# Optimization experiments

Hardware: AMD Instinct MI355X
Metric: run time of the kernel (lower is better)

## Reference

```python
import jax, jax.numpy as jnp
import numpy as np

DT_MIN, DT_MAX = 1e-3, 0.1
DT_RANK, D_STATE, D_CONV = 64, 16, 4


def setup_inputs() -> dict:
    key = jax.random.key(0)
    ks = jax.random.split(key, 8)
    B, T, Dm = 4, 4096, 1024
    Dn = 2 * Dm  # expand * d_model
    s = lambda k, shape, scale=0.02: (jax.random.normal(k, shape, jnp.float32) * scale)
    return {
        "x": jax.random.normal(ks[0], (B, T, Dm), jnp.float32),
        "W_in": s(ks[1], (2 * Dn, Dm)),
        "conv_w": s(ks[2], (Dn, 1, D_CONV), 0.1),
        "conv_b": jnp.zeros((Dn,), jnp.float32),
        "W_x": s(ks[3], (DT_RANK + 2 * D_STATE, Dn)),
        "W_dt": s(ks[4], (Dn, DT_RANK)),
        "b_dt": jnp.zeros((Dn,), jnp.float32),
        "log_A": jax.random.uniform(ks[5], (Dn, D_STATE), jnp.float32),
        "D_param": jnp.ones((Dn,), jnp.float32),
        "W_out": s(ks[6], (Dm, Dn)),
        "ln_w": jnp.ones((Dm,), jnp.float32),
        "ln_b": jnp.zeros((Dm,), jnp.float32),
    }


def reference(x, W_in, conv_w, conv_b, W_x, W_dt, b_dt, log_A, D_param, W_out, ln_w, ln_b):
    B, T, Dm = x.shape
    Dn = W_dt.shape[0]
    residual = x
    # LayerNorm (biased variance, eps=1e-5, as torch)
    mu = x.mean(-1, keepdims=True)
    var = x.var(-1, keepdims=True)
    xn = (x - mu) / jnp.sqrt(var + 1e-5) * ln_w + ln_b
    # in_proj -> split into x_inner, z
    xz = xn @ W_in.T  # (B,T,2*Dn)
    x_inner, z = jnp.split(xz, 2, axis=-1)
    # causal depthwise conv (torch pads both sides d_conv-1 then slices [:T] == left-pad only)
    xc = jnp.transpose(x_inner, (0, 2, 1))  # (B,Dn,T)
    xc = jax.lax.conv_general_dilated(
        xc, conv_w, window_strides=(1,), padding=[(D_CONV - 1, 0)],
        dimension_numbers=("NCH", "OIH", "NCH"), feature_group_count=Dn)
    xc = xc + conv_b[None, :, None]
    u = jax.nn.silu(jnp.transpose(xc, (0, 2, 1)))  # (B,T,Dn)
    # input-dependent dt, B, C
    xbc = u @ W_x.T
    dt_low, B_ssm, C_ssm = jnp.split(xbc, [DT_RANK, DT_RANK + D_STATE], axis=-1)
    dt = jax.nn.softplus(dt_low @ W_dt.T + b_dt) + DT_MIN
    dt = jnp.clip(dt, DT_MIN, DT_MAX)  # (B,T,Dn)
    A = -jnp.exp(log_A)  # (Dn,N), always negative -> stable
    # selective scan: h_t = exp(dt*A)*h_{t-1} + (dt*u)*B_t ; y_t = <C_t, h_t>
    def step(h, inp):
        dt_t, u_t, B_t, C_t = inp  # (B,Dn),(B,Dn),(B,N),(B,N)
        dA = jnp.exp(dt_t[:, :, None] * A)  # (B,Dn,N)
        h = dA * h + (dt_t * u_t)[:, :, None] * B_t[:, None, :]
        y = jnp.einsum("bdn,bn->bd", h, C_t)
        return h, y

    h0 = jnp.zeros((B, Dn, D_STATE), x.dtype)
    _, ys = jax.lax.scan(
        step, h0,
        (jnp.moveaxis(dt, 1, 0), jnp.moveaxis(u, 1, 0),
         jnp.moveaxis(B_ssm, 1, 0), jnp.moveaxis(C_ssm, 1, 0)))
    y = jnp.moveaxis(ys, 0, 1)  # (B,T,Dn)
    y = y + u * D_param
    y = y * jax.nn.silu(z)
    return y @ W_out.T + residual
```

## Files before the change

kernel.cpp:

```cpp
#include <hip/hip_runtime.h>
#include <cstdint>
#include <cstddef>

#define TT 4096
#define DM 1024
#define DN 2048
#define MROWS 16384
#define NCH 64
#define CHL 64
#define SW 16
#define XBCS 128

typedef unsigned short u16;
typedef u16 ushort8_t __attribute__((ext_vector_type(8)));
typedef u16 ushort4_t __attribute__((ext_vector_type(4)));
typedef short bf16x8 __attribute__((ext_vector_type(8)));
typedef float f32x4 __attribute__((ext_vector_type(4)));

#define EXP2(x) __builtin_amdgcn_exp2f(x)
#define L2E 1.44269504f

__device__ __forceinline__ float bf2f(u16 b) {
  return __uint_as_float(((unsigned int)b) << 16);
}
__device__ __forceinline__ u16 f2bf(float f) {
  unsigned int u = __float_as_uint(f);
  u = u + 0x7FFFu + ((u >> 16) & 1u);
  return (u16)(u >> 16);
}
__device__ __forceinline__ u16 f2h(float f) {
  _Float16 h = (_Float16)f;
  return __builtin_bit_cast(u16, h);
}
__device__ __forceinline__ float h2f(u16 v) {
  return (float)__builtin_bit_cast(_Float16, v);
}

__device__ __forceinline__ void gload_lds16(const void* g, void* l) {
  __builtin_amdgcn_global_load_lds(
      (const __attribute__((address_space(1))) unsigned int*)g,
      (__attribute__((address_space(3))) unsigned int*)l, 16, 0, 0);
}

#define FENCE() asm volatile("" ::: "memory")

__global__ __launch_bounds__(256) void cvt_bf16_kernel(const float* __restrict__ in,
    u16* __restrict__ out, int n4) {
  int i = blockIdx.x * 256 + threadIdx.x;
  if (i >= n4) return;
  float4 v = ((const float4*)in)[i];
  ushort4_t o; o[0] = f2bf(v.x); o[1] = f2bf(v.y); o[2] = f2bf(v.z); o[3] = f2bf(v.w);
  ((ushort4_t*)out)[i] = o;
}

__global__ __launch_bounds__(256) void cvt_wx_kernel(const float* __restrict__ W_x,
    u16* __restrict__ out) {
  int i = blockIdx.x * 256 + threadIdx.x;
  int row = i >> 9;
  ushort4_t o;
  if (row < 96) {
    float4 v = ((const float4*)W_x)[i];
    o[0] = f2bf(v.x); o[1] = f2bf(v.y); o[2] = f2bf(v.z); o[3] = f2bf(v.w);
  } else {
    o[0] = 0; o[1] = 0; o[2] = 0; o[3] = 0;
  }
  ((ushort4_t*)out)[i] = o;
}

__global__ __launch_bounds__(256) void ln_kernel(const float* __restrict__ x,
    const float* __restrict__ ln_w, const float* __restrict__ ln_b,
    u16* __restrict__ xn) {
  int row = blockIdx.x;
  int tid = threadIdx.x;
  const float4* xr = (const float4*)(x + (size_t)row * DM);
  float4 v = xr[tid];
  float s  = v.x + v.y + v.z + v.w;
  float s2 = v.x*v.x + v.y*v.y + v.z*v.z + v.w*v.w;
#pragma unroll
  for (int o = 32; o > 0; o >>= 1) { s += __shfl_down(s, o, 64); s2 += __shfl_down(s2, o, 64); }
  __shared__ float red[2][4];
  __shared__ float mv[2];
  int wid = tid >> 6, lane = tid & 63;
  if (lane == 0) { red[0][wid] = s; red[1][wid] = s2; }
  __syncthreads();
  if (tid == 0) {
    float a  = red[0][0] + red[0][1] + red[0][2] + red[0][3];
    float b2 = red[1][0] + red[1][1] + red[1][2] + red[1][3];
    float mean = a * (1.f / DM);
    float var  = b2 * (1.f / DM) - mean * mean;
    mv[0] = mean; mv[1] = rsqrtf(var + 1e-5f);
  }
  __syncthreads();
  float mean = mv[0], inv = mv[1];
  float4 w = ((const float4*)ln_w)[tid];
  float4 b = ((const float4*)ln_b)[tid];
  ushort4_t o;
  o[0] = f2bf((v.x - mean) * inv * w.x + b.x);
  o[1] = f2bf((v.y - mean) * inv * w.y + b.y);
  o[2] = f2bf((v.z - mean) * inv * w.z + b.z);
  o[3] = f2bf((v.w - mean) * inv * w.w + b.w);
  *(ushort4_t*)(xn + (size_t)row * DM + tid * 4) = o;
}

template<int MODE>
__global__ __launch_bounds__(256) void gemm_mfma_nt(
    const u16* __restrict__ A, int lda,
    const u16* __restrict__ B, int ldb,
    void* __restrict__ Cp, int ldc,
    const float* __restrict__ Res, int K,
    const float* __restrict__ bias, u16* __restrict__ dl_out) {
  __shared__ __align__(16) u16 a_s[128 * 64];
  __shared__ __align__(16) u16 b_s[128 * 64];
  const int tid = threadIdx.x;
  const int w = tid >> 6, l = tid & 63;
  const int wr = w >> 1, wc = w & 1;
  const int nbx = gridDim.x, gy = gridDim.y;
  int lin = blockIdx.y * nbx + blockIdx.x;
  int xcd = lin & 7;
  int m = lin >> 3;
  int bi, bj;
  if (gy >= 8) {
    int njx = gy >> 3;
    bi = m / njx;
    bj = xcd * njx + m % njx;
  } else {
    int cpx = (nbx * gy) >> 3;
    int swz = xcd * cpx + m;
    bi = swz % nbx; bj = swz / nbx;
  }
  const int lrow = l >> 3;
  const int scol = ((l & 7) ^ lrow) * 16;

  f32x4 acc[4][4] = {};

  const int brow = (MODE == 4) ? 0 : bj;
  const u16* Abase = A + (size_t)(bi * 128 + w * 8 + lrow) * lda;
  const u16* Bbase = B + (size_t)(brow * 128 + w * 8 + lrow) * ldb;

  int kbeg = 0, kend = K;
  if constexpr (MODE == 4) { kbeg = bj * (K >> 1); kend = kbeg + (K >> 1); }
  for (int k0 = kbeg; k0 < kend; k0 += 64) {
#pragma unroll
    for (int c = 0; c < 4; c++) {
      const char* ga = (const char*)(Abase + (size_t)(c * 32) * lda + k0) + scol;
      const char* gb = (const char*)(Bbase + (size_t)(c * 32) * ldb + k0) + scol;
      gload_lds16(ga, (char*)a_s + c * 4096 + w * 1024);
      gload_lds16(gb, (char*)b_s + c * 4096 + w * 1024);
    }
    __syncthreads();
#pragma unroll
    for (int kk = 0; kk < 2; kk++) {
      bf16x8 af[4], bfr[4];
#pragma unroll
      for (int m2 = 0; m2 < 4; m2++) {
        int fr = wr * 64 + m2 * 16 + (l & 15);
        int cb = (kk * 64 + ((l >> 4) << 4)) ^ ((fr & 7) << 4);
        af[m2] = *(const bf16x8*)((const char*)a_s + fr * 128 + cb);
      }
#pragma unroll
      for (int n = 0; n < 4; n++) {
        int fr = wc * 64 + n * 16 + (l & 15);
        int cb = (kk * 64 + ((l >> 4) << 4)) ^ ((fr & 7) << 4);
        bfr[n] = *(const bf16x8*)((const char*)b_s + fr * 128 + cb);
      }
#pragma unroll
      for (int m2 = 0; m2 < 4; m2++)
#pragma unroll
        for (int n = 0; n < 4; n++)
          acc[m2][n] = __builtin_amdgcn_mfma_f32_16x16x32_bf16(af[m2], bfr[n], acc[m2][n], 0, 0, 0);
    }
    __syncthreads();
  }
  const int col0 = ((MODE == 4) ? 0 : bj * 128) + wc * 64 + (l & 15);
  const int row0 = bi * 128 + wr * 64 + (l >> 4) * 4;
#pragma unroll
  for (int m2 = 0; m2 < 4; m2++)
#pragma unroll
    for (int n = 0; n < 4; n++) {
      int col = col0 + n * 16;
      float bv = 0.f;
      if constexpr (MODE == 3) bv = bias[col];
#pragma unroll
      for (int r = 0; r < 4; r++) {
        size_t row = (size_t)(row0 + m2 * 16 + r);
        float v = acc[m2][n][r];
        if constexpr (MODE == 0) {
          ((u16*)Cp)[row * ldc + col] = f2bf(v);
        } else if constexpr (MODE == 2) {
          v += Res[row * ldc + col];
          ((float*)Cp)[row * ldc + col] = v;
        } else if constexpr (MODE == 4) {
          ((float*)Cp)[(size_t)bj * ((size_t)MROWS * 128) + row * ldc + col] = v;
        } else {
          float s = v + bv;
          float sp = __logf(1.f + __expf(s));
          float dtv = fminf(sp + 1e-3f, 0.1f);
          ((u16*)Cp)[row * ldc + col] = f2h(dtv);
        }
      }
    }
}

__global__ __launch_bounds__(256) void xbc_merge(const float* __restrict__ p0,
    const float* __restrict__ p1, float* __restrict__ xbc, u16* __restrict__ dl) {
  int i = blockIdx.x * 256 + threadIdx.x;
  float4 a = ((const float4*)p0)[i];
  float4 b = ((const float4*)p1)[i];
  float4 s; s.x = a.x + b.x; s.y = a.y + b.y; s.z = a.z + b.z; s.w = a.w + b.w;
  ((float4*)xbc)[i] = s;
  int col = (i & 31) * 4;
  if (col < 64) {
    int row = i >> 5;
    ushort4_t o; o[0] = f2bf(s.x); o[1] = f2bf(s.y); o[2] = f2bf(s.z); o[3] = f2bf(s.w);
    *(ushort4_t*)(dl + (size_t)row * 64 + col) = o;
  }
}

template<int MODE>
__global__ __launch_bounds__(512) void gemm256(
    const u16* __restrict__ A, int lda,
    const u16* __restrict__ B, int ldb,
    void* __restrict__ Cp, int ldc,
    const float* __restrict__ Res, int K) {
  extern __shared__ char smem[];
  const int tid = threadIdx.x;
  const int w = tid >> 6, l = tid & 63;
  const int wm = w >> 2, wn = w & 3;
  const int nbx = gridDim.x, gy = gridDim.y;
  int lin = blockIdx.y * nbx + blockIdx.x;
  int xcd = lin & 7, mm = lin >> 3;
  int bi, bj;
  if (gy >= 8) { int njx = gy >> 3; bi = mm / njx; bj = xcd * njx + mm % njx; }
  else { int cpx = (nbx * gy) >> 3; int swz = xcd * cpx + mm; bi = swz % nbx; bj = swz / nbx; }
  const int lrow = l >> 3;
  const int scol = ((l & 7) ^ lrow) * 16;
  const int l15 = l & 15, lhi = (l >> 4) << 4;
  const u16* aRow = A + (size_t)(bi * 256 + w * 8 + lrow) * lda;
  const u16* bRow = B + (size_t)(bj * 256 + w * 8 + lrow) * ldb;
  char* As = smem;
  char* Bs = smem + 65536;

#define IS_A(s, k) gload_lds16((const char*)(aRow + (size_t)((k) * 64) * lda + (size_t)(s) * 64) + scol, \
                               As + ((((s) & 1)) << 15) + (k) * 8192 + w * 1024)
#define IS_B(s, k) gload_lds16((const char*)(bRow + (size_t)((k) * 64) * ldb + (size_t)(s) * 64) + scol, \
                               Bs + ((((s) & 1)) << 15) + (k) * 8192 + w * 1024)

  f32x4 acc[8][4] = {};
  bf16x8 bf[2][4];
  const int NT = K >> 6;

  IS_B(0, 0); IS_B(0, 1); IS_B(0, 2); IS_B(0, 3);
  IS_A(0, 0); IS_A(0, 2); IS_A(0, 1); IS_A(0, 3);
  IS_B(1, 0); IS_B(1, 1); IS_B(1, 2); IS_B(1, 3); IS_A(1, 0);

#define MFMA8(MLO, KK) do { \
    bf16x8 a0_ = ardA(MLO, KK), a1_ = ardA((MLO) + 1, KK); \
    __builtin_amdgcn_s_setprio(1); \
    _Pragma("unroll") \
    for (int n_ = 0; n_ < 4; n_++) { \
      acc[MLO][n_]       = __builtin_amdgcn_mfma_f32_16x16x32_bf16(a0_, bf[KK][n_], acc[MLO][n_], 0, 0, 0); \
      acc[(MLO) + 1][n_] = __builtin_amdgcn_mfma_f32_16x16x32_bf16(a1_, bf[KK][n_], acc[(MLO) + 1][n_], 0, 0, 0); \
    } \
    __builtin_amdgcn_s_setprio(0); \
  } while (0)

  for (int t = 0; t < NT; ++t) {
    const char* Ab = As + ((t & 1) << 15);
    const char* Bb = Bs + ((t & 1) << 15);
    auto ardA = [&](int m, int kk) {
      int fr = wm * 128 + m * 16 + l15;
      int cb = (kk * 64 + lhi) ^ ((fr & 7) << 4);
      return *(const bf16x8*)(Ab + fr * 128 + cb);
    };
    auto ardB = [&](int n, int kk) {
      int fr = wn * 64 + n * 16 + l15;
      int cb = (kk * 64 + lhi) ^ ((fr & 7) << 4);
      return *(const bf16x8*)(Bb + fr * 128 + cb);
    };
    if (t + 1 < NT) IS_A(t + 1, 2);
    FENCE();
    asm volatile("s_waitcnt vmcnt(8)" ::: "memory");
    __builtin_amdgcn_s_barrier();
    FENCE();
    bf[0][0] = ardB(0, 0); bf[0][1] = ardB(1, 0); bf[0][2] = ardB(2, 0); bf[0][3] = ardB(3, 0);
    MFMA8(0, 0);
    if (t + 1 < NT) IS_A(t + 1, 1);
    MFMA8(2, 0);
    if (t + 1 < NT) IS_A(t + 1, 3);
    bf[1][0] = ardB(0, 1); bf[1][1] = ardB(1, 1); bf[1][2] = ardB(2, 1); bf[1][3] = ardB(3, 1);
    MFMA8(0, 1);
    FENCE();
    __builtin_amdgcn_s_barrier();
    FENCE();
    if (t + 2 < NT) IS_B(t + 2, 0);
    MFMA8(2, 1);
    if (t + 2 < NT) IS_B(t + 2, 1);
    FENCE();
    asm volatile("s_waitcnt vmcnt(10)" ::: "memory");
    __builtin_amdgcn_s_barrier();
    FENCE();
    MFMA8(4, 0);
    if (t + 2 < NT) IS_B(t + 2, 2);
    MFMA8(6, 0);
    if (t + 2 < NT) IS_B(t + 2, 3);
    MFMA8(4, 1);
    if (t + 2 < NT) IS_A(t + 2, 0);
    MFMA8(6, 1);
  }
#undef MFMA8
#undef IS_A
#undef IS_B

  const int col0 = bj * 256 + wn * 64 + l15;
  const int row0 = bi * 256 + wm * 128 + (l >> 4) * 4;
#pragma unroll
  for (int m = 0; m < 8; m++)
#pragma unroll
    for (int n = 0; n < 4; n++) {
      int col = col0 + n * 16;
#pragma unroll
      for (int r = 0; r < 4; r++) {
        size_t row = (size_t)(row0 + m * 16 + r);
        float v = acc[m][n][r];
        if constexpr (MODE == 0) {
          ((u16*)Cp)[row * ldc + col] = f2bf(v);
        } else {
          v += Res[row * ldc + col];
          ((float*)Cp)[row * ldc + col] = v;
        }
      }
    }
}

__global__ __launch_bounds__(256) void conv_silu_kernel(const u16* __restrict__ xz,
    const float* __restrict__ conv_w, const float* __restrict__ conv_b,
    u16* __restrict__ u) {
  size_t gid = (size_t)blockIdx.x * 256 + threadIdx.x;
  int c = (int)(gid & 255);
  size_t i = gid >> 8;
  int t = (int)(i & (TT - 1));
  int d0 = c * 8;
  const u16* base = xz + i * 4096 + d0;
  ushort8_t r0 = *(const ushort8_t*)base;
  ushort8_t r1 = 0, r2 = 0, r3 = 0;
  if (t >= 1) r1 = *(const ushort8_t*)(base - 4096);
  if (t >= 2) r2 = *(const ushort8_t*)(base - 2 * 4096);
  if (t >= 3) r3 = *(const ushort8_t*)(base - 3 * 4096);
  float cbv[8];
  *(float4*)&cbv[0] = *(const float4*)(conv_b + d0);
  *(float4*)&cbv[4] = *(const float4*)(conv_b + d0 + 4);
  ushort8_t o;
#pragma unroll
  for (int j = 0; j < 8; j++) {
    float4 w = *(const float4*)(conv_w + (size_t)(d0 + j) * 4);
    float a = cbv[j] + w.w * bf2f(r0[j]) + w.z * bf2f(r1[j])
            + w.y * bf2f(r2[j]) + w.x * bf2f(r3[j]);
    a = a * __builtin_amdgcn_rcpf(1.f + EXP2(-a * L2E));
    o[j] = f2bf(a);
  }
  *(ushort8_t*)(u + i * 2048 + d0) = o;
}

__global__ __launch_bounds__(256) void scan_part1(u16* u_g,
    const u16* __restrict__ dt_g, const float* __restrict__ xbc,
    const float* __restrict__ log_A, const float* __restrict__ D_param,
    float* __restrict__ hbuf, float* __restrict__ Sbuf) {
  int d0 = blockIdx.x * 128;
  int c  = blockIdx.y;
  int b  = blockIdx.z;
  int tid = threadIdx.x;
  int w = tid >> 6, l = tid & 63;
  int dl = tid >> 1, q = tid & 1, q8 = q << 3;
  int d = d0 + dl;
  __shared__ __align__(16) u16 u_s[2][SW][128];
  __shared__ __align__(16) u16 dts[2][SW][128];
  __shared__ __align__(16) float bc_s[2][SW][32];

  float A2[8];
  {
    float4 la0 = *(const float4*)(log_A + (size_t)d * 16 + q8);
    float4 la1 = *(const float4*)(log_A + (size_t)d * 16 + q8 + 4);
    A2[0] = -EXP2(la0.x * L2E) * L2E; A2[1] = -EXP2(la0.y * L2E) * L2E;
    A2[2] = -EXP2(la0.z * L2E) * L2E; A2[3] = -EXP2(la0.w * L2E) * L2E;
    A2[4] = -EXP2(la1.x * L2E) * L2E; A2[5] = -EXP2(la1.y * L2E) * L2E;
    A2[6] = -EXP2(la1.z * L2E) * L2E; A2[7] = -EXP2(la1.w * L2E) * L2E;
  }
  float Dp = D_param[d];
  float h[8] = {};
  float sdt = 0.f;
  size_t t0 = (size_t)b * TT + (size_t)c * CHL;
  const int sr = w * 4 + (l >> 4);
  const int sc = (l & 15) * 8;
  u16* up = u_g + t0 * 2048 + d;

#define P1STAGE(wnd, pb) { size_t i0_ = t0 + (size_t)(wnd) * SW;                          \
    gload_lds16(u_g  + (i0_ + sr) * 2048 + d0 + sc, (char*)u_s[pb] + w * 1024);           \
    gload_lds16(dt_g + (i0_ + sr) * 4096 + d0 + sc, (char*)dts[pb] + w * 1024);           \
    if (w < 2) gload_lds16(xbc + (i0_ + w * 8 + (l >> 3)) * XBCS + 64 + (l & 7) * 4,      \
                           (char*)bc_s[pb] + w * 1024); }

  P1STAGE(0, 0);
  for (int wnd = 0; wnd < CHL / SW; wnd++) {
    int pb = wnd & 1;
    __syncthreads();
    if (wnd + 1 < CHL / SW) P1STAGE(wnd + 1, pb ^ 1);
#pragma unroll 4
    for (int tt = 0; tt < SW; tt++) {
      float dtv = h2f(dts[pb][tt][dl]);
      float uv  = bf2f(u_s[pb][tt][dl]);
      sdt += dtv;
      float xin = dtv * uv;
      float yv = q ? 0.f : uv * Dp;
      float4 B0 = *(const float4*)&bc_s[pb][tt][q8];
      float4 B1 = *(const float4*)&bc_s[pb][tt][q8 + 4];
      float4 C0 = *(const float4*)&bc_s[pb][tt][16 + q8];
      float4 C1 = *(const float4*)&bc_s[pb][tt][16 + q8 + 4];
      h[0] = __builtin_fmaf(EXP2(dtv * A2[0]), h[0], xin * B0.x); yv = __builtin_fmaf(h[0], C0.x, yv);
      h[1] = __builtin_fmaf(EXP2(dtv * A2[1]), h[1], xin * B0.y); yv = __builtin_fmaf(h[1], C0.y, yv);
      h[2] = __builtin_fmaf(EXP2(dtv * A2[2]), h[2], xin * B0.z); yv = __builtin_fmaf(h[2], C0.z, yv);
      h[3] = __builtin_fmaf(EXP2(dtv * A2[3]), h[3], xin * B0.w); yv = __builtin_fmaf(h[3], C0.w, yv);
      h[4] = __builtin_fmaf(EXP2(dtv * A2[4]), h[4], xin * B1.x); yv = __builtin_fmaf(h[4], C1.x, yv);
      h[5] = __builtin_fmaf(EXP2(dtv * A2[5]), h[5], xin * B1.y); yv = __builtin_fmaf(h[5], C1.y, yv);
      h[6] = __builtin_fmaf(EXP2(dtv * A2[6]), h[6], xin * B1.z); yv = __builtin_fmaf(h[6], C1.z, yv);
      h[7] = __builtin_fmaf(EXP2(dtv * A2[7]), h[7], xin * B1.w); yv = __builtin_fmaf(h[7], C1.w, yv);
      yv += __shfl_xor(yv, 1, 64);
      if (q == 0) *up = f2h(yv);
      up += 2048;
    }
  }
  float* hp = hbuf + (((size_t)b * NCH + c) * 16 + q8) * DN + d;
#pragma unroll
  for (int k = 0; k < 8; k++) hp[(size_t)k * DN] = h[k];
  if (q == 0) Sbuf[((size_t)b * NCH + c) * DN + d] = sdt;
#undef P1STAGE
}

__global__ __launch_bounds__(256) void scan_combine(const float* __restrict__ log_A,
    const float* __restrict__ Sbuf, float* __restrict__ hbuf) {
  int idx = blockIdx.x * 256 + threadIdx.x;
  int dd = idx & (DN - 1), n = (idx >> 11) & 15, b = idx >> 15;
  float A2 = -EXP2(log_A[(size_t)dd * 16 + n] * L2E) * L2E;
  float h = 0.f;
#pragma unroll
  for (int c = 0; c < NCH; c++) {
    size_t off = (((size_t)b * NCH + c) * 16 + n) * DN + dd;
    float hl = hbuf[off];
    float P = EXP2(A2 * Sbuf[((size_t)b * NCH + c) * DN + dd]);
    hbuf[off] = h;
    h = hl + P * h;
  }
}

__global__ __launch_bounds__(256) void scan_part2(u16* yl,
    const u16* __restrict__ xz, const float* __restrict__ xbc,
    const u16* __restrict__ dt_g, const float* __restrict__ log_A,
    const float* __restrict__ hbuf) {
  int d0 = blockIdx.x * 128;
  int c  = blockIdx.y;
  int b  = blockIdx.z;
  int tid = threadIdx.x;
  int w = tid >> 6, l = tid & 63;
  int dl = tid >> 1, q = tid & 1, q8 = q << 3;
  int d = d0 + dl;
  __shared__ __align__(16) u16 yls[2][SW][128];
  __shared__ __align__(16) u16 z_s[2][SW][128];
  __shared__ __align__(16) u16 dts[2][SW][128];
  __shared__ __align__(16) float c_s[2][SW][16];

  float A2[8];
  {
    float4 la0 = *(const float4*)(log_A + (size_t)d * 16 + q8);
    float4 la1 = *(const float4*)(log_A + (size_t)d * 16 + q8 + 4);
    A2[0] = -EXP2(la0.x * L2E) * L2E; A2[1] = -EXP2(la0.y * L2E) * L2E;
    A2[2] = -EXP2(la0.z * L2E) * L2E; A2[3] = -EXP2(la0.w * L2E) * L2E;
    A2[4] = -EXP2(la1.x * L2E) * L2E; A2[5] = -EXP2(la1.y * L2E) * L2E;
    A2[6] = -EXP2(la1.z * L2E) * L2E; A2[7] = -EXP2(la1.w * L2E) * L2E;
  }
  float hs[8];
  {
    const float* hp = hbuf + (((size_t)b * NCH + c) * 16 + q8) * DN + d;
#pragma unroll
    for (int k = 0; k < 8; k++) hs[k] = hp[(size_t)k * DN];
  }
  float cum = 0.f;
  size_t t0 = (size_t)b * TT + (size_t)c * CHL;
  const int sr = w * 4 + (l >> 4);
  const int sc = (l & 15) * 8;
  u16* ylp = yl + t0 * 2048 + d;

#define P2STAGE(wnd, pb) { size_t i0_ = t0 + (size_t)(wnd) * SW;                          \
    gload_lds16(yl   + (i0_ + sr) * 2048 + d0 + sc, (char*)yls[pb] + w * 1024);           \
    gload_lds16(xz   + (i0_ + sr) * 4096 + 2048 + d0 + sc, (char*)z_s[pb] + w * 1024);    \
    gload_lds16(dt_g + (i0_ + sr) * 4096 + d0 + sc, (char*)dts[pb] + w * 1024);           \
    if (w == 0) gload_lds16(xbc + (i0_ + (l >> 2)) * XBCS + 80 + (l & 3) * 4,             \
                            (char*)c_s[pb]); }

  P2STAGE(0, 0);
  for (int wnd = 0; wnd < CHL / SW; wnd++) {
    int pb = wnd & 1;
    __syncthreads();
    if (wnd + 1 < CHL / SW) P2STAGE(wnd + 1, pb ^ 1);
#pragma unroll 4
    for (int tt = 0; tt < SW; tt++) {
      float dtv = h2f(dts[pb][tt][dl]);
      cum += dtv;
      float4 C0 = *(const float4*)&c_s[pb][tt][q8];
      float4 C1 = *(const float4*)&c_s[pb][tt][q8 + 4];
      float yv = C0.x * (EXP2(cum * A2[0]) * hs[0]) + C0.y * (EXP2(cum * A2[1]) * hs[1])
               + C0.z * (EXP2(cum * A2[2]) * hs[2]) + C0.w * (EXP2(cum * A2[3]) * hs[3])
               + C1.x * (EXP2(cum * A2[4]) * hs[4]) + C1.y * (EXP2(cum * A2[5]) * hs[5])
               + C1.z * (EXP2(cum * A2[6]) * hs[6]) + C1.w * (EXP2(cum * A2[7]) * hs[7]);
      if (q == 0) yv += h2f(yls[pb][tt][dl]);
      yv += __shfl_xor(yv, 1, 64);
      float zv = bf2f(z_s[pb][tt][dl]);
      float sig = __builtin_amdgcn_rcpf(1.f + EXP2(-zv * L2E));
      if (q == 0) *ylp = f2bf(yv * zv * sig);
      ylp += 2048;
    }
  }
#undef P2STAGE
}

extern "C" void kernel_launch(void* const* d_in, const int* in_sizes, int n_in,
                              void* d_out, int out_size, void* d_ws, size_t ws_size,
                              hipStream_t stream) {
  const float* x       = (const float*)d_in[0];
  const float* W_in    = (const float*)d_in[1];
  const float* conv_w  = (const float*)d_in[2];
  const float* conv_b  = (const float*)d_in[3];
  const float* W_x     = (const float*)d_in[4];
  const float* W_dt    = (const float*)d_in[5];
  const float* b_dt    = (const float*)d_in[6];
  const float* log_A   = (const float*)d_in[7];
  const float* D_param = (const float*)d_in[8];
  const float* W_out   = (const float*)d_in[9];
  const float* ln_w    = (const float*)d_in[10];
  const float* ln_b    = (const float*)d_in[11];
  float* out = (float*)d_out;

  size_t need = (size_t)MROWS * 4096 * 2 + (size_t)MROWS * DN * 2 + (size_t)MROWS * 96 * 4;
  if (ws_size < need) return;
  u16*   xz  = (u16*)d_ws;
  u16*   u   = xz + (size_t)MROWS * 4096;
  u16*   W_out_b = (u16*)(u + (size_t)MROWS * DN);

  u16*   xn_b    = (u16*)d_out;
  float* xbc_p   = (float*)d_out;
  float* xbc     = (float*)d_out;
  float* hbuf    = (float*)((char*)d_out + (8u << 20));
  u16*   W_in_b  = (u16*)((char*)d_out + (40u << 20));
  float* Sbuf    = (float*)((char*)d_out + (48u << 20));
  u16*   W_x_b   = (u16*)((char*)d_out + (50u << 20));
  u16*   W_dt_b  = (u16*)((char*)d_out + (50u << 20) + (512u << 10));
  u16*   dl_b    = (u16*)((char*)d_out + (51u << 20));

  static int use256 = -1;
  if (use256 < 0) {
    hipError_t e0 = hipFuncSetAttribute(reinterpret_cast<const void*>(&gemm256<0>),
        hipFuncAttributeMaxDynamicSharedMemorySize, 131072);
    hipError_t e2 = hipFuncSetAttribute(reinterpret_cast<const void*>(&gemm256<2>),
        hipFuncAttributeMaxDynamicSharedMemorySize, 131072);
    use256 = (e0 == hipSuccess && e2 == hipSuccess) ? 1 : 0;
  }

  cvt_wx_kernel<<<(128 * 2048 / 4) / 256, 256, 0, stream>>>(W_x, W_x_b);
  cvt_bf16_kernel<<<(2048 * 64 / 4) / 256, 256, 0, stream>>>(W_dt, W_dt_b, 2048 * 64 / 4);
  ln_kernel<<<MROWS, 256, 0, stream>>>(x, ln_w, ln_b, xn_b);
  cvt_bf16_kernel<<<(4096 * 1024 / 4) / 256, 256, 0, stream>>>(W_in, W_in_b, 4096 * 1024 / 4);
  if (use256) {
    gemm256<0><<<dim3(MROWS / 256, 4096 / 256), 512, 131072, stream>>>(
        xn_b, DM, W_in_b, DM, xz, 4096, nullptr, DM);
  } else {
    gemm_mfma_nt<0><<<dim3(MROWS / 128, 4096 / 128), 256, 0, stream>>>(
        xn_b, DM, W_in_b, DM, xz, 4096, nullptr, DM, nullptr, nullptr);
  }
  conv_silu_kernel<<<MROWS, 256, 0, stream>>>(xz, conv_w, conv_b, u);
  gemm_mfma_nt<4><<<dim3(MROWS / 128, 2), 256, 0, stream>>>(
      u, DN, W_x_b, DN, xbc_p, XBCS, nullptr, DN, nullptr, nullptr);
  xbc_merge<<<(MROWS * 128 / 4) / 256, 256, 0, stream>>>(
      xbc_p, xbc_p + (size_t)MROWS * 128, xbc, dl_b);
  gemm_mfma_nt<3><<<dim3(MROWS / 128, DN / 128), 256, 0, stream>>>(
      dl_b, 64, W_dt_b, 64, xz, 4096, nullptr, 64, b_dt, nullptr);
  scan_part1<<<dim3(DN / 128, NCH, 4), 256, 0, stream>>>(
      u, xz, xbc, log_A, D_param, hbuf, Sbuf);
  scan_combine<<<4 * DN * 16 / 256, 256, 0, stream>>>(log_A, Sbuf, hbuf);
  scan_part2<<<dim3(DN / 128, NCH, 4), 256, 0, stream>>>(
      u, xz, xbc, xz, log_A, hbuf);
  cvt_bf16_kernel<<<(1024 * 2048 / 4) / 256, 256, 0, stream>>>(W_out, W_out_b, 1024 * 2048 / 4);
  if (use256) {
    gemm256<2><<<dim3(MROWS / 256, 1024 / 256), 512, 131072, stream>>>(
        u, DN, W_out_b, DN, out, DM, x, DN);
  } else {
    gemm_mfma_nt<2><<<dim3(MROWS / 128, 1024 / 128), 256, 0, stream>>>(
        u, DN, W_out_b, DN, out, DM, x, DN, nullptr, nullptr);
  }
}
```

Baseline: 603.5 us.

## Fuse weight conversions, split xbc GEMM 4-way, fp16 scan states, nontemporal epilogue

Merges the three weight-to-bf16 conversion launches into one kernel. Splits the K dimension of the x->(dt,B,C) GEMM into four partial sums instead of two, which raises the number of blocks, and merges the four partials in xbc_merge. Stores the inter-chunk scan states in fp16 instead of fp32 to halve that traffic, and uses nontemporal loads and stores for the residual epilogue of the output GEMMs. The fp16 hidden states may lose precision, and the four-way split means more partial-sum traffic.

```diff
diff --git a/kernel.cpp b/kernel.cpp
--- a/kernel.cpp
+++ b/kernel.cpp
@@ -53,18 +53,33 @@
   ((ushort4_t*)out)[i] = o;
 }
 
-__global__ __launch_bounds__(256) void cvt_wx_kernel(const float* __restrict__ W_x,
-    u16* __restrict__ out) {
-  int i = blockIdx.x * 256 + threadIdx.x;
-  int row = i >> 9;
-  ushort4_t o;
-  if (row < 96) {
-    float4 v = ((const float4*)W_x)[i];
-    o[0] = f2bf(v.x); o[1] = f2bf(v.y); o[2] = f2bf(v.z); o[3] = f2bf(v.w);
+__global__ __launch_bounds__(256) void cvt_weights_kernel(
+    const float* __restrict__ W_in, u16* __restrict__ W_in_b,
+    const float* __restrict__ W_x, u16* __restrict__ W_x_b,
+    const float* __restrict__ W_dt, u16* __restrict__ W_dt_b) {
+  int b = blockIdx.x, t = threadIdx.x;
+  if (b < 4096) {
+    int i = b * 256 + t;
+    float4 v = ((const float4*)W_in)[i];
+    ushort4_t o; o[0] = f2bf(v.x); o[1] = f2bf(v.y); o[2] = f2bf(v.z); o[3] = f2bf(v.w);
+    ((ushort4_t*)W_in_b)[i] = o;
+  } else if (b < 4352) {
+    int i = (b - 4096) * 256 + t;
+    int row = i >> 9;
+    ushort4_t o;
+    if (row < 96) {
+      float4 v = ((const float4*)W_x)[i];
+      o[0] = f2bf(v.x); o[1] = f2bf(v.y); o[2] = f2bf(v.z); o[3] = f2bf(v.w);
+    } else {
+      o[0] = 0; o[1] = 0; o[2] = 0; o[3] = 0;
+    }
+    ((ushort4_t*)W_x_b)[i] = o;
   } else {
-    o[0] = 0; o[1] = 0; o[2] = 0; o[3] = 0;
-  }
-  ((ushort4_t*)out)[i] = o;
+    int i = (b - 4352) * 256 + t;
+    float4 v = ((const float4*)W_dt)[i];
+    ushort4_t o; o[0] = f2bf(v.x); o[1] = f2bf(v.y); o[2] = f2bf(v.z); o[3] = f2bf(v.w);
+    ((ushort4_t*)W_dt_b)[i] = o;
+  }
 }
 
 __global__ __launch_bounds__(256) void ln_kernel(const float* __restrict__ x,
@@ -138,7 +153,7 @@
   const u16* Bbase = B + (size_t)(brow * 128 + w * 8 + lrow) * ldb;
 
   int kbeg = 0, kend = K;
-  if constexpr (MODE == 4) { kbeg = bj * (K >> 1); kend = kbeg + (K >> 1); }
+  if constexpr (MODE == 4) { kbeg = bj * (K >> 2); kend = kbeg + (K >> 2); }
   for (int k0 = kbeg; k0 < kend; k0 += 64) {
 #pragma unroll
     for (int c = 0; c < 4; c++) {
@@ -187,8 +202,8 @@
         if constexpr (MODE == 0) {
           ((u16*)Cp)[row * ldc + col] = f2bf(v);
         } else if constexpr (MODE == 2) {
-          v += Res[row * ldc + col];
-          ((float*)Cp)[row * ldc + col] = v;
+          v += __builtin_nontemporal_load(&Res[row * ldc + col]);
+          __builtin_nontemporal_store(v, &((float*)Cp)[row * ldc + col]);
         } else if constexpr (MODE == 4) {
           ((float*)Cp)[(size_t)bj * ((size_t)MROWS * 128) + row * ldc + col] = v;
         } else {
@@ -201,12 +216,19 @@
     }
 }
 
-__global__ __launch_bounds__(256) void xbc_merge(const float* __restrict__ p0,
-    const float* __restrict__ p1, float* __restrict__ xbc, u16* __restrict__ dl) {
+__global__ __launch_bounds__(256) void xbc_merge(const float* __restrict__ p,
+    float* __restrict__ xbc, u16* __restrict__ dl) {
   int i = blockIdx.x * 256 + threadIdx.x;
-  float4 a = ((const float4*)p0)[i];
-  float4 b = ((const float4*)p1)[i];
-  float4 s; s.x = a.x + b.x; s.y = a.y + b.y; s.z = a.z + b.z; s.w = a.w + b.w;
+  const size_t PS = (size_t)MROWS * 128 / 4;
+  float4 a = ((const float4*)p)[i];
+  float4 b = ((const float4*)p)[i + PS];
+  float4 c = ((const float4*)p)[i + 2 * PS];
+  float4 d = ((const float4*)p)[i + 3 * PS];
+  float4 s;
+  s.x = (a.x + b.x) + (c.x + d.x);
+  s.y = (a.y + b.y) + (c.y + d.y);
+  s.z = (a.z + b.z) + (c.z + d.z);
+  s.w = (a.w + b.w) + (c.w + d.w);
   ((float4*)xbc)[i] = s;
   int col = (i & 31) * 4;
   if (col < 64) {
@@ -325,8 +347,8 @@
         if constexpr (MODE == 0) {
           ((u16*)Cp)[row * ldc + col] = f2bf(v);
         } else {
-          v += Res[row * ldc + col];
-          ((float*)Cp)[row * ldc + col] = v;
+          v += __builtin_nontemporal_load(&Res[row * ldc + col]);
+          __builtin_nontemporal_store(v, &((float*)Cp)[row * ldc + col]);
         }
       }
     }
@@ -364,7 +386,7 @@
 __global__ __launch_bounds__(256) void scan_part1(u16* u_g,
     const u16* __restrict__ dt_g, const float* __restrict__ xbc,
     const float* __restrict__ log_A, const float* __restrict__ D_param,
-    float* __restrict__ hbuf, float* __restrict__ Sbuf) {
+    u16* __restrict__ hbuf, float* __restrict__ Sbuf) {
   int d0 = blockIdx.x * 128;
   int c  = blockIdx.y;
   int b  = blockIdx.z;
@@ -428,15 +450,15 @@
       up += 2048;
     }
   }
-  float* hp = hbuf + (((size_t)b * NCH + c) * 16 + q8) * DN + d;
-#pragma unroll
-  for (int k = 0; k < 8; k++) hp[(size_t)k * DN] = h[k];
+  u16* hp = hbuf + (((size_t)b * NCH + c) * 16 + q8) * DN + d;
+#pragma unroll
+  for (int k = 0; k < 8; k++) hp[(size_t)k * DN] = f2h(h[k]);
   if (q == 0) Sbuf[((size_t)b * NCH + c) * DN + d] = sdt;
 #undef P1STAGE
 }
 
 __global__ __launch_bounds__(256) void scan_combine(const float* __restrict__ log_A,
-    const float* __restrict__ Sbuf, float* __restrict__ hbuf) {
+    const float* __restrict__ Sbuf, u16* __restrict__ hbuf) {
   int idx = blockIdx.x * 256 + threadIdx.x;
   int dd = idx & (DN - 1), n = (idx >> 11) & 15, b = idx >> 15;
   float A2 = -EXP2(log_A[(size_t)dd * 16 + n] * L2E) * L2E;
@@ -444,9 +466,9 @@
 #pragma unroll
   for (int c = 0; c < NCH; c++) {
     size_t off = (((size_t)b * NCH + c) * 16 + n) * DN + dd;
-    float hl = hbuf[off];
+    float hl = h2f(hbuf[off]);
     float P = EXP2(A2 * Sbuf[((size_t)b * NCH + c) * DN + dd]);
-    hbuf[off] = h;
+    hbuf[off] = f2h(h);
     h = hl + P * h;
   }
 }
@@ -454,7 +476,7 @@
 __global__ __launch_bounds__(256) void scan_part2(u16* yl,
     const u16* __restrict__ xz, const float* __restrict__ xbc,
     const u16* __restrict__ dt_g, const float* __restrict__ log_A,
-    const float* __restrict__ hbuf) {
+    const u16* __restrict__ hbuf) {
   int d0 = blockIdx.x * 128;
   int c  = blockIdx.y;
   int b  = blockIdx.z;
@@ -478,9 +500,9 @@
   }
   float hs[8];
   {
-    const float* hp = hbuf + (((size_t)b * NCH + c) * 16 + q8) * DN + d;
-#pragma unroll
-    for (int k = 0; k < 8; k++) hs[k] = hp[(size_t)k * DN];
+    const u16* hp = hbuf + (((size_t)b * NCH + c) * 16 + q8) * DN + d;
+#pragma unroll
+    for (int k = 0; k < 8; k++) hs[k] = h2f(hp[(size_t)k * DN]);
   }
   float cum = 0.f;
   size_t t0 = (size_t)b * TT + (size_t)c * CHL;
@@ -547,7 +569,7 @@
   u16*   xn_b    = (u16*)d_out;
   float* xbc_p   = (float*)d_out;
   float* xbc     = (float*)d_out;
-  float* hbuf    = (float*)((char*)d_out + (8u << 20));
+  u16*   hbuf    = (u16*)((char*)d_out + (32u << 20));
   u16*   W_in_b  = (u16*)((char*)d_out + (40u << 20));
   float* Sbuf    = (float*)((char*)d_out + (48u << 20));
   u16*   W_x_b   = (u16*)((char*)d_out + (50u << 20));
@@ -563,10 +585,8 @@
     use256 = (e0 == hipSuccess && e2 == hipSuccess) ? 1 : 0;
   }
 
-  cvt_wx_kernel<<<(128 * 2048 / 4) / 256, 256, 0, stream>>>(W_x, W_x_b);
-  cvt_bf16_kernel<<<(2048 * 64 / 4) / 256, 256, 0, stream>>>(W_dt, W_dt_b, 2048 * 64 / 4);
+  cvt_weights_kernel<<<4480, 256, 0, stream>>>(W_in, W_in_b, W_x, W_x_b, W_dt, W_dt_b);
   ln_kernel<<<MROWS, 256, 0, stream>>>(x, ln_w, ln_b, xn_b);
-  cvt_bf16_kernel<<<(4096 * 1024 / 4) / 256, 256, 0, stream>>>(W_in, W_in_b, 4096 * 1024 / 4);
   if (use256) {
     gemm256<0><<<dim3(MROWS / 256, 4096 / 256), 512, 131072, stream>>>(
         xn_b, DM, W_in_b, DM, xz, 4096, nullptr, DM);
@@ -575,10 +595,9 @@
         xn_b, DM, W_in_b, DM, xz, 4096, nullptr, DM, nullptr, nullptr);
   }
   conv_silu_kernel<<<MROWS, 256, 0, stream>>>(xz, conv_w, conv_b, u);
-  gemm_mfma_nt<4><<<dim3(MROWS / 128, 2), 256, 0, stream>>>(
+  gemm_mfma_nt<4><<<dim3(MROWS / 128, 4), 256, 0, stream>>>(
       u, DN, W_x_b, DN, xbc_p, XBCS, nullptr, DN, nullptr, nullptr);
-  xbc_merge<<<(MROWS * 128 / 4) / 256, 256, 0, stream>>>(
-      xbc_p, xbc_p + (size_t)MROWS * 128, xbc, dl_b);
+  xbc_merge<<<(MROWS * 128 / 4) / 256, 256, 0, stream>>>(xbc_p, xbc, dl_b);
   gemm_mfma_nt<3><<<dim3(MROWS / 128, DN / 128), 256, 0, stream>>>(
       dl_b, 64, W_dt_b, 64, xz, 4096, nullptr, 64, b_dt, nullptr);
   scan_part1<<<dim3(DN / 128, NCH, 4), 256, 0, stream>>>(
```

Result: no change. 598.9 us (-0.8%).
